# Kernel tuning notes

Hardware: AMD Instinct MI355X
Metric: run time of the kernel (lower is better)

The kernel has to match this reference:

```python
import jax, jax.numpy as jnp
import numpy as np
from jax import lax

N_ITER = 100          # max_iter=100 in forward's sparse_fit call
EPS = 1e-8            # multiplicative-update denominator guard
H_IMG, W_IMG = 1024, 1024
R2 = 4                # self.r = r*2 with default r=2


def setup_inputs() -> dict:
    key = jax.random.key(0)
    k1, k2, k3, k4, k5 = jax.random.split(key, 5)
    N = H_IMG * W_IMG
    pic = jax.random.uniform(k1, (3, H_IMG, W_IMG), jnp.float32)            # source RGB image in [0,1]
    W_target = jax.random.uniform(k2, (3, R2), jnp.float32, 0.05, 1.0)      # target stain matrix (nmft.H)
    Ht_RM = jax.random.uniform(k3, (), jnp.float32, 0.5, 2.0)               # 0.99-quantile of target concentrations
    W0 = jax.random.uniform(k4, (N, R2), jnp.float32, 0.05, 1.0)            # NMF concentration init (torchnmf W)
    H0 = jax.random.uniform(k5, (3, R2), jnp.float32, 0.05, 1.0)            # NMF stain-matrix init (torchnmf H)
    return {"pic": pic, "W_target": W_target, "Ht_RM": Ht_RM, "W0": W0, "H0": H0}


def _nmf_fit(V, H0, W0):
    # V (3,N) ~= Hd @ Wc.T ; Hd (3,r) stain matrix, Wc (N,r) concentrations.
    # Standard beta=2 (Frobenius) multiplicative updates, N_ITER iterations.
    def step(carry, _):
        Hd, Wc = carry
        Wc = Wc * (V.T @ Hd) / (Wc @ (Hd.T @ Hd) + EPS)   # (N,r): skinny GEMMs via r x r Gram
        Hd = Hd * (V @ Wc) / (Hd @ (Wc.T @ Wc) + EPS)     # (3,r)
        return (Hd, Wc), None

    (Hd, Wc), _ = lax.scan(jax.checkpoint(step), (H0, W0), None, length=N_ITER)
    return Hd, Wc


def reference(pic, W_target, Ht_RM, W0, H0):
    c, h, w = pic.shape
    V = -jnp.log(jnp.clip(pic.reshape(3, -1), 0.01, 0.99))   # optical density, (3,N)
    Hd, Wc = _nmf_fit(V, H0, W0)
    H_s = Wc.T                                               # (r,N) source concentrations
    H_sn = H_s * Ht_RM / jnp.quantile(H_s, 0.99)             # quantile normalization to target
    out = jnp.exp(-(W_target @ H_sn)).reshape(c, h, w)       # recompose with target stains
    return jnp.clip(out, 0.0, 1.0)
```

## Files before the change

### kernel.cpp

```cpp
#include <hip/hip_runtime.h>
#include <math.h>


#define N_PIX (1024*1024)
#define NB    256
#define BS    512
#define NWAVE (BS/64)
#define TT    (NB*BS)
#define PPT   (N_PIX/TT)
#define NIT   100
#define EPSI  1e-8f
#define NBINS 2048
#define TSTR  24
#define SSTR  24

#define OFF_GH0_B 0
#define OFF_GH1_B 8192
#define OFF_T1_B  16384
#define OFF_T2_B  (16384 + NB*2*TSTR*8)
#define WS_BYTES  (OFF_T2_B + NB*2*TSTR*8)

typedef unsigned long long u64;

__device__ __forceinline__ u64 ld_tag(const u64* p) {
    return __hip_atomic_load(p, __ATOMIC_RELAXED, __HIP_MEMORY_SCOPE_AGENT);
}
__device__ __forceinline__ void st_tag(u64* p, u64 v) {
    __hip_atomic_store(p, v, __ATOMIC_RELAXED, __HIP_MEMORY_SCOPE_AGENT);
}
__device__ __forceinline__ unsigned ld_rlx_u(const unsigned* p) {
    return __hip_atomic_load(p, __ATOMIC_RELAXED, __HIP_MEMORY_SCOPE_AGENT);
}
__device__ __forceinline__ u64 pack_tag(unsigned ep, float x) {
    return ((u64)ep << 32) | (u64)__float_as_uint(x);
}
__device__ __forceinline__ float spin_fast(const u64* p, unsigned ep) {
    const u64 thr = ((u64)ep) << 32;
    u64 v = ld_tag(p);
    while (v < thr) v = ld_tag(p);
    return __uint_as_float((unsigned)v);
}
__device__ __forceinline__ float spin_val(const u64* p, unsigned ep) {
    const u64 thr = ((u64)ep) << 32;
    u64 v = ld_tag(p);
    while (v < thr) { __builtin_amdgcn_s_sleep(1); v = ld_tag(p); }
    return __uint_as_float((unsigned)v);
}
__device__ __forceinline__ void spin_only(const u64* p, unsigned ep) {
    const u64 thr = ((u64)ep) << 32;
    while (ld_tag(p) < thr) __builtin_amdgcn_s_sleep(1);
}

__global__ __launch_bounds__(BS)
void he_norm_kernel(const float* __restrict__ pic,
                    const float* __restrict__ Wt,
                    const float* __restrict__ HtRM,
                    const float* __restrict__ W0,
                    const float* __restrict__ H0,
                    float* __restrict__ out,
                    unsigned char* __restrict__ ws)
{
    const int tid  = threadIdx.x;
    const int blk  = blockIdx.x;
    const int g    = blk*BS + tid;
    const int wave = tid >> 6;
    const int lane = tid & 63;
    const int rowB = blk & ~15;
    const int col  = blk & 15;

    unsigned* gh0 = (unsigned*)(ws + OFF_GH0_B);
    unsigned* gh1 = (unsigned*)(ws + OFF_GH1_B);
    u64*      T1  = (u64*)(ws + OFF_T1_B);
    u64*      T2  = (u64*)(ws + OFF_T2_B);

    __shared__ float sAcc[BS*SSTR];
    __shared__ float sPrA[16][22];
    __shared__ float sPrB[16][22];
    __shared__ float sWv[NWAVE*32];
    __shared__ float sWt[12], sScal[2];
    __shared__ float sRed[NWAVE][2];
    __shared__ unsigned sHist[NBINS];
    __shared__ unsigned sSeg[256];
    __shared__ int      sBstar;
    __shared__ unsigned sCumB;

    if (tid < 12) sWt[tid] = Wt[tid];
    float hd[12], gg[16];
    #pragma unroll
    for (int j = 0; j < 12; j++) hd[j] = H0[j];
    #pragma unroll
    for (int j = 0; j < 16; j++) {
        int s_ = j >> 2, r_ = j & 3;
        gg[j] = hd[s_]*hd[r_] + hd[4+s_]*hd[4+r_] + hd[8+s_]*hd[8+r_];
    }

    float v0[PPT], v1[PPT], v2[PPT];
    float w[PPT][4];
    #pragma unroll
    for (int k = 0; k < PPT; k++) {
        int i = g + k*TT;
        float4 wv = ((const float4*)W0)[i];
        w[k][0]=wv.x; w[k][1]=wv.y; w[k][2]=wv.z; w[k][3]=wv.w;
        v0[k] = -logf(fminf(fmaxf(pic[i],           0.01f), 0.99f));
        v1[k] = -logf(fminf(fmaxf(pic[N_PIX  + i],  0.01f), 0.99f));
        v2[k] = -logf(fminf(fmaxf(pic[2*N_PIX + i], 0.01f), 0.99f));
    }
    __syncthreads();

    for (int t = 0; t < NIT; ++t) {
        float acc[22];
        #pragma unroll
        for (int j = 0; j < 22; j++) acc[j] = 0.f;

        #pragma unroll
        for (int k = 0; k < PPT; k++) {
            float wn[4];
            #pragma unroll
            for (int r = 0; r < 4; r++) {
                float num = v0[k]*hd[r] + v1[k]*hd[4+r] + v2[k]*hd[8+r];
                float den = w[k][0]*gg[r] + w[k][1]*gg[4+r]
                          + w[k][2]*gg[8+r] + w[k][3]*gg[12+r] + EPSI;
                float rc = __builtin_amdgcn_rcpf(den);
                rc = rc * (2.0f - den*rc);
                wn[r] = w[k][r] * num * rc;
            }
            #pragma unroll
            for (int r = 0; r < 4; r++) {
                acc[r]    += v0[k]*wn[r];
                acc[4+r]  += v1[k]*wn[r];
                acc[8+r]  += v2[k]*wn[r];
            }
            acc[12]+=wn[0]*wn[0]; acc[13]+=wn[0]*wn[1]; acc[14]+=wn[0]*wn[2]; acc[15]+=wn[0]*wn[3];
            acc[16]+=wn[1]*wn[1]; acc[17]+=wn[1]*wn[2]; acc[18]+=wn[1]*wn[3];
            acc[19]+=wn[2]*wn[2]; acc[20]+=wn[2]*wn[3]; acc[21]+=wn[3]*wn[3];
            w[k][0]=wn[0]; w[k][1]=wn[1]; w[k][2]=wn[2]; w[k][3]=wn[3];
        }

        if (t == NIT-1) break;
        const unsigned ep  = (unsigned)(t + 1);
        const int      par = (int)(ep & 1u);

        {
            float4* dst = (float4*)&sAcc[tid*SSTR];
            dst[0] = make_float4(acc[0], acc[1], acc[2], acc[3]);
            dst[1] = make_float4(acc[4], acc[5], acc[6], acc[7]);
            dst[2] = make_float4(acc[8], acc[9], acc[10], acc[11]);
            dst[3] = make_float4(acc[12], acc[13], acc[14], acc[15]);
            dst[4] = make_float4(acc[16], acc[17], acc[18], acc[19]);
            *((float2*)&sAcc[tid*SSTR + 20]) = make_float2(acc[20], acc[21]);
        }
        __syncthreads();
        if (tid < 352) {
            int seg = tid / 22, j = tid - seg*22;
            const float* row = &sAcc[(seg*32)*SSTR + j];
            float p0=0.f, p1=0.f, p2=0.f, p3=0.f;
            #pragma unroll
            for (int b = 0; b < 32; b += 4) {
                p0 += row[(b+0)*SSTR]; p1 += row[(b+1)*SSTR];
                p2 += row[(b+2)*SSTR]; p3 += row[(b+3)*SSTR];
            }
            sPrA[seg][j] = (p0+p1)+(p2+p3);
        }
        __syncthreads();
        if (tid < 22) {
            float bp = 0.f;
            #pragma unroll
            for (int sg = 0; sg < 16; sg++) bp += sPrA[sg][tid];
            st_tag(&T1[(blk*2 + par)*TSTR + tid], pack_tag(ep, bp));
        }

        if (tid < 352) {
            int m = tid / 22, j = tid - m*22;
            sPrB[m][j] = spin_fast(&T1[((rowB + m)*2 + par)*TSTR + j], ep);
        }
        __syncthreads();
        if (tid < 22) {
            float rs = 0.f;
            #pragma unroll
            for (int m = 0; m < 16; m++) rs += sPrB[m][tid];
            st_tag(&T2[(blk*2 + par)*TSTR + tid], pack_tag(ep, rs));
        }

        if (tid < 352) {
            int m = tid / 22, j = tid - m*22;
            sPrA[m][j] = spin_fast(&T2[((m*16 + col)*2 + par)*TSTR + j], ep);
        }
        __syncthreads();

        {
            if (lane < 22) {
                float s = 0.f;
                #pragma unroll
                for (int m = 0; m < 16; m++) s += sPrA[m][lane];
                sWv[wave*32 + lane] = s;
            }
            float ss[22];
            {
                const float4* wr = (const float4*)&sWv[wave*32];
                float4 a0 = wr[0], a1 = wr[1], a2 = wr[2], a3 = wr[3], a4 = wr[4];
                float2 a5 = ((const float2*)&sWv[wave*32])[10];
                ss[0]=a0.x; ss[1]=a0.y; ss[2]=a0.z; ss[3]=a0.w;
                ss[4]=a1.x; ss[5]=a1.y; ss[6]=a1.z; ss[7]=a1.w;
                ss[8]=a2.x; ss[9]=a2.y; ss[10]=a2.z; ss[11]=a2.w;
                ss[12]=a3.x; ss[13]=a3.y; ss[14]=a3.z; ss[15]=a3.w;
                ss[16]=a4.x; ss[17]=a4.y; ss[18]=a4.z; ss[19]=a4.w;
                ss[20]=a5.x; ss[21]=a5.y;
            }
            float nhd[12];
            const int base[4] = {12, 16, 19, 21};
            #pragma unroll
            for (int c = 0; c < 3; c++)
                #pragma unroll
                for (int r = 0; r < 4; r++) {
                    float den = EPSI;
                    #pragma unroll
                    for (int s2 = 0; s2 < 4; s2++) {
                        int lo = (s2 < r) ? s2 : r, hi = (s2 < r) ? r : s2;
                        den += hd[c*4 + s2] * ss[base[lo] + (hi - lo)];
                    }
                    nhd[c*4+r] = hd[c*4+r] * ss[c*4+r] / den;
                }
            #pragma unroll
            for (int j = 0; j < 12; j++) hd[j] = nhd[j];
            #pragma unroll
            for (int j = 0; j < 16; j++) {
                int s_ = j >> 2, r_ = j & 3;
                gg[j] = hd[s_]*hd[r_] + hd[4+s_]*hd[4+r_] + hd[8+s_]*hd[8+r_];
            }
        }
    }

    {
        float m = 0.f;
        #pragma unroll
        for (int k = 0; k < PPT; k++)
            #pragma unroll
            for (int r = 0; r < 4; r++) m = fmaxf(m, w[k][r]);
        #pragma unroll
        for (int off = 32; off > 0; off >>= 1) m = fmaxf(m, __shfl_down(m, off, 64));
        if (lane == 0) sRed[wave][0] = m;
        __syncthreads();
        if (tid == 0) {
            float mm = 0.f;
            for (int wv2 = 0; wv2 < NWAVE; wv2++) mm = fmaxf(mm, sRed[wv2][0]);
            st_tag(&T1[(blk*2 + 0)*TSTR + 0], pack_tag(100u, mm));
        }
        if (tid < NB) sAcc[tid] = spin_val(&T1[(tid*2 + 0)*TSTR + 0], 100u);
        __syncthreads();
        if (tid < NB) {
            float mv = sAcc[tid];
            #pragma unroll
            for (int off = 32; off > 0; off >>= 1) mv = fmaxf(mv, __shfl_down(mv, off, 64));
            if (lane == 0) sRed[wave][1] = mv;
        }
        __syncthreads();
        if (tid == 0) {
            float mm = 0.f;
            for (int wv2 = 0; wv2 < 4; wv2++) mm = fmaxf(mm, sRed[wv2][1]);
            sScal[0] = mm * 1.0000002f;
        }
        __syncthreads();
    }
    const float gmax   = sScal[0];
    const float scale0 = (float)NBINS / gmax;

    for (int i = tid; i < NBINS; i += BS) sHist[i] = 0u;
    __syncthreads();
    #pragma unroll
    for (int k = 0; k < PPT; k++)
        #pragma unroll
        for (int r = 0; r < 4; r++) {
            int b = (int)(w[k][r] * scale0);
            b = min(b, NBINS - 1);
            atomicAdd(&sHist[b], 1u);
        }
    __syncthreads();
    for (int i = tid; i < NBINS; i += BS) if (sHist[i]) atomicAdd(&gh0[i], sHist[i]);
    __builtin_amdgcn_s_waitcnt(0);
    __syncthreads();
    if (tid == 0) st_tag(&T1[(blk*2 + 1)*TSTR + 0], pack_tag(101u, 0.f));
    if (tid < NB) spin_only(&T1[(tid*2 + 1)*TSTR + 0], 101u);
    __syncthreads();

    const double kfd = 0.99 * (double)(4*N_PIX - 1);
    if (tid < 256) {
        unsigned s2 = 0;
        for (int i = 0; i < 8; i++) s2 += ld_rlx_u(&gh0[tid*8 + i]);
        sSeg[tid] = s2;
    }
    __syncthreads();
    if (tid == 0) {
        unsigned cum = 0; int seg = 0;
        for (int i2 = 0; i2 < 256; i2++) {
            if ((double)(cum + sSeg[i2]) > kfd) { seg = i2; break; }
            cum += sSeg[i2];
        }
        unsigned c2 = cum; int b = seg*8;
        for (int i2 = 0; i2 < 8; i2++) {
            unsigned h = ld_rlx_u(&gh0[seg*8 + i2]);
            if ((double)(c2 + h) > kfd) { b = seg*8 + i2; break; }
            c2 += h;
        }
        sBstar = b; sCumB = c2;
    }
    __syncthreads();
    const int   bstar  = sBstar;
    const float lo1    = (float)bstar / scale0;
    const float scale1 = scale0 * (float)NBINS;

    for (int i = tid; i < NBINS; i += BS) sHist[i] = 0u;
    __syncthreads();
    #pragma unroll
    for (int k = 0; k < PPT; k++)
        #pragma unroll
        for (int r = 0; r < 4; r++) {
            int b0 = min((int)(w[k][r] * scale0), NBINS - 1);
            if (b0 == bstar) {
                int b1 = (int)((w[k][r] - lo1) * scale1);
                b1 = max(0, min(b1, NBINS - 1));
                atomicAdd(&sHist[b1], 1u);
            }
        }
    __syncthreads();
    for (int i = tid; i < NBINS; i += BS) if (sHist[i]) atomicAdd(&gh1[i], sHist[i]);
    __builtin_amdgcn_s_waitcnt(0);
    __syncthreads();
    if (tid == 0) st_tag(&T1[(blk*2 + 0)*TSTR + 0], pack_tag(102u, 0.f));
    if (tid < NB) spin_only(&T1[(tid*2 + 0)*TSTR + 0], 102u);
    __syncthreads();

    if (tid < 256) {
        unsigned s2 = 0;
        for (int i = 0; i < 8; i++) s2 += ld_rlx_u(&gh1[tid*8 + i]);
        sSeg[tid] = s2;
    }
    __syncthreads();
    if (tid == 0) {
        double jf = kfd - (double)sCumB;
        unsigned cum = 0; int seg = 0;
        for (int i2 = 0; i2 < 256; i2++) {
            if ((double)(cum + sSeg[i2]) > jf) { seg = i2; break; }
            cum += sSeg[i2];
        }
        unsigned c3 = cum; int bb = seg*8; unsigned hh = 1;
        for (int i2 = 0; i2 < 8; i2++) {
            unsigned h = ld_rlx_u(&gh1[seg*8 + i2]);
            if ((double)(c3 + h) > jf) { bb = seg*8 + i2; hh = h; break; }
            c3 += h;
        }
        double frac = (jf - (double)c3 + 0.5) / (double)hh;
        frac = fmin(fmax(frac, 0.0), 1.0);
        double q = (double)lo1 + ((double)bb + frac) / (double)scale1;
        sScal[1] = (float)((double)HtRM[0] / q);
    }
    __syncthreads();
    const float sc = sScal[1];

    #pragma unroll
    for (int k = 0; k < PPT; k++) {
        int i = g + k*TT;
        #pragma unroll
        for (int c = 0; c < 3; c++) {
            float d = sWt[c*4+0]*w[k][0] + sWt[c*4+1]*w[k][1]
                    + sWt[c*4+2]*w[k][2] + sWt[c*4+3]*w[k][3];
            float e = expf(-d * sc);
            out[c*N_PIX + i] = fminf(fmaxf(e, 0.f), 1.f);
        }
    }
}

extern "C" void kernel_launch(void* const* d_in, const int* in_sizes, int n_in,
                              void* d_out, int out_size, void* d_ws, size_t ws_size,
                              hipStream_t stream) {
    const float* pic  = (const float*)d_in[0];
    const float* Wt   = (const float*)d_in[1];
    const float* HtRM = (const float*)d_in[2];
    const float* W0   = (const float*)d_in[3];
    const float* H0   = (const float*)d_in[4];
    float* out = (float*)d_out;

    hipMemsetAsync(d_ws, 0, WS_BYTES, stream);
    he_norm_kernel<<<dim3(NB), dim3(BS), 0, stream>>>(
        pic, Wt, HtRM, W0, H0, out, (unsigned char*)d_ws);
}
```

Measured before the change: 661.8 us.

## Replace all-to-all transpose reduction with group-leader two-level grid reduction

Changes the per-iteration cross-block reduction of the 22 partial sums. Previously every block polled its 16 row neighbours, then 16 column partials, spinning without sleeping. Now one leader block per group of 16 polls its members, writes a single group partial, and every block reads the 16 group partials with a sleeping spin. This cuts global tag traffic and polling contention, but puts the leader's serial gather on the critical path. Separately, the shared staging stride moves from 24 to 23 to avoid LDS bank conflicts, which gives up the vectorised float4 stores and loads.

```diff
diff --git a/kernel.cpp b/kernel.cpp
--- a/kernel.cpp
+++ b/kernel.cpp
@@ -11,14 +11,15 @@
 #define NIT   100
 #define EPSI  1e-8f
 #define NBINS 2048
+#define NGRP  16
 #define TSTR  24
-#define SSTR  24
+#define SSTR  23
 
 #define OFF_GH0_B 0
 #define OFF_GH1_B 8192
 #define OFF_T1_B  16384
 #define OFF_T2_B  (16384 + NB*2*TSTR*8)
-#define WS_BYTES  (OFF_T2_B + NB*2*TSTR*8)
+#define WS_BYTES  (OFF_T2_B + NGRP*2*TSTR*8)
 
 typedef unsigned long long u64;
 
@@ -33,12 +34,6 @@
 }
 __device__ __forceinline__ u64 pack_tag(unsigned ep, float x) {
     return ((u64)ep << 32) | (u64)__float_as_uint(x);
-}
-__device__ __forceinline__ float spin_fast(const u64* p, unsigned ep) {
-    const u64 thr = ((u64)ep) << 32;
-    u64 v = ld_tag(p);
-    while (v < thr) v = ld_tag(p);
-    return __uint_as_float((unsigned)v);
 }
 __device__ __forceinline__ float spin_val(const u64* p, unsigned ep) {
     const u64 thr = ((u64)ep) << 32;
@@ -65,8 +60,9 @@
     const int g    = blk*BS + tid;
     const int wave = tid >> 6;
     const int lane = tid & 63;
-    const int rowB = blk & ~15;
-    const int col  = blk & 15;
+    const int grp  = blk >> 4;
+    const int isLeader = ((blk & 15) == 0);
+    const int grpBase  = grp << 4;
 
     unsigned* gh0 = (unsigned*)(ws + OFF_GH0_B);
     unsigned* gh1 = (unsigned*)(ws + OFF_GH1_B);
@@ -76,7 +72,7 @@
     __shared__ float sAcc[BS*SSTR];
     __shared__ float sPrA[16][22];
     __shared__ float sPrB[16][22];
-    __shared__ float sWv[NWAVE*32];
+    __shared__ float sWv[NWAVE*24];
     __shared__ float sWt[12], sScal[2];
     __shared__ float sRed[NWAVE][2];
     __shared__ unsigned sHist[NBINS];
@@ -140,15 +136,8 @@
         const unsigned ep  = (unsigned)(t + 1);
         const int      par = (int)(ep & 1u);
 
-        {
-            float4* dst = (float4*)&sAcc[tid*SSTR];
-            dst[0] = make_float4(acc[0], acc[1], acc[2], acc[3]);
-            dst[1] = make_float4(acc[4], acc[5], acc[6], acc[7]);
-            dst[2] = make_float4(acc[8], acc[9], acc[10], acc[11]);
-            dst[3] = make_float4(acc[12], acc[13], acc[14], acc[15]);
-            dst[4] = make_float4(acc[16], acc[17], acc[18], acc[19]);
-            *((float2*)&sAcc[tid*SSTR + 20]) = make_float2(acc[20], acc[21]);
-        }
+        #pragma unroll
+        for (int j = 0; j < 22; j++) sAcc[tid*SSTR + j] = acc[j];
         __syncthreads();
         if (tid < 352) {
             int seg = tid / 22, j = tid - seg*22;
@@ -169,21 +158,28 @@
             st_tag(&T1[(blk*2 + par)*TSTR + tid], pack_tag(ep, bp));
         }
 
+        if (isLeader && wave == 0 && lane < 22) {
+            const u64 thr = ((u64)ep) << 32;
+            u64 v[16];
+            for (;;) {
+                bool ok = true;
+                #pragma unroll
+                for (int m = 0; m < 16; m++)
+                    v[m] = ld_tag(&T1[((grpBase + m)*2 + par)*TSTR + lane]);
+                #pragma unroll
+                for (int m = 0; m < 16; m++) ok &= (v[m] >= thr);
+                if (ok) break;
+                __builtin_amdgcn_s_sleep(1);
+            }
+            float gp = 0.f;
+            #pragma unroll
+            for (int m = 0; m < 16; m++) gp += __uint_as_float((unsigned)v[m]);
+            st_tag(&T2[(grp*2 + par)*TSTR + lane], pack_tag(ep, gp));
+        }
+
         if (tid < 352) {
-            int m = tid / 22, j = tid - m*22;
-            sPrB[m][j] = spin_fast(&T1[((rowB + m)*2 + par)*TSTR + j], ep);
-        }
-        __syncthreads();
-        if (tid < 22) {
-            float rs = 0.f;
-            #pragma unroll
-            for (int m = 0; m < 16; m++) rs += sPrB[m][tid];
-            st_tag(&T2[(blk*2 + par)*TSTR + tid], pack_tag(ep, rs));
-        }
-
-        if (tid < 352) {
-            int m = tid / 22, j = tid - m*22;
-            sPrA[m][j] = spin_fast(&T2[((m*16 + col)*2 + par)*TSTR + j], ep);
+            int g2 = tid / 22, j = tid - g2*22;
+            sPrB[g2][j] = spin_val(&T2[(g2*2 + par)*TSTR + j], ep);
         }
         __syncthreads();
 
@@ -191,21 +187,12 @@
             if (lane < 22) {
                 float s = 0.f;
                 #pragma unroll
-                for (int m = 0; m < 16; m++) s += sPrA[m][lane];
-                sWv[wave*32 + lane] = s;
+                for (int m = 0; m < 16; m++) s += sPrB[m][lane];
+                sWv[wave*24 + lane] = s;
             }
             float ss[22];
-            {
-                const float4* wr = (const float4*)&sWv[wave*32];
-                float4 a0 = wr[0], a1 = wr[1], a2 = wr[2], a3 = wr[3], a4 = wr[4];
-                float2 a5 = ((const float2*)&sWv[wave*32])[10];
-                ss[0]=a0.x; ss[1]=a0.y; ss[2]=a0.z; ss[3]=a0.w;
-                ss[4]=a1.x; ss[5]=a1.y; ss[6]=a1.z; ss[7]=a1.w;
-                ss[8]=a2.x; ss[9]=a2.y; ss[10]=a2.z; ss[11]=a2.w;
-                ss[12]=a3.x; ss[13]=a3.y; ss[14]=a3.z; ss[15]=a3.w;
-                ss[16]=a4.x; ss[17]=a4.y; ss[18]=a4.z; ss[19]=a4.w;
-                ss[20]=a5.x; ss[21]=a5.y;
-            }
+            #pragma unroll
+            for (int j = 0; j < 22; j++) ss[j] = sWv[wave*24 + j];
             float nhd[12];
             const int base[4] = {12, 16, 19, 21};
             #pragma unroll
```

Result: slower. 685.3 us (+3.6%).
